# Kernel optimization log

Measured on AMD Instinct MI355X. Metric: run time of the kernel, lower is better.

## Reference

```python
import jax, jax.numpy as jnp
import numpy as np

B, N, CS, CZ, CH, H, PQ, PV = 1, 768, 384, 128, 16, 12, 4, 8
INF, EPS = 1e5, 1e-8


def quat_to_rot(q):
    q = q / jnp.linalg.norm(q, axis=-1, keepdims=True)
    w, x, y, z = q[..., 0], q[..., 1], q[..., 2], q[..., 3]
    r0 = jnp.stack([1 - 2 * (y * y + z * z), 2 * (x * y - w * z), 2 * (x * z + w * y)], -1)
    r1 = jnp.stack([2 * (x * y + w * z), 1 - 2 * (x * x + z * z), 2 * (y * z - w * x)], -1)
    r2 = jnp.stack([2 * (x * z - w * y), 2 * (y * z + w * x), 1 - 2 * (x * x + y * y)], -1)
    return jnp.stack([r0, r1, r2], -2)


def setup_inputs() -> dict:
    key = jax.random.key(0)
    ks = jax.random.split(key, 12)
    nrm = lambda k, shp, sc=1.0: jax.random.normal(k, shp, jnp.float32) * sc
    s = nrm(ks[0], (B, N, CS))
    z = nrm(ks[1], (B, N, N, CZ))
    rot = quat_to_rot(nrm(ks[2], (B, N, 4)))
    trans = nrm(ks[3], (B, N, 3))
    mask = jnp.ones((B, N), jnp.float32)
    dout = H * (CZ + CH + PV * 4)
    return dict(
        s=s, z=z, rot=rot, trans=trans, mask=mask,
        w_q=nrm(ks[4], (H * CH, CS), 0.02), b_q=jnp.zeros((H * CH,), jnp.float32),
        w_kv=nrm(ks[5], (2 * H * CH, CS), 0.02), b_kv=jnp.zeros((2 * H * CH,), jnp.float32),
        w_qp=nrm(ks[6], (H * PQ * 3, CS), 0.02), b_qp=jnp.zeros((H * PQ * 3,), jnp.float32),
        w_kvp=nrm(ks[7], (H * (PQ + PV) * 3, CS), 0.02), b_kvp=jnp.zeros((H * (PQ + PV) * 3,), jnp.float32),
        w_b=nrm(ks[8], (H, CZ), 0.02), b_b=jnp.zeros((H,), jnp.float32),
        head_weights=jnp.full((H,), 0.541324854612918, jnp.float32),
        w_out=nrm(ks[9], (CS, dout), 0.02), b_out=jnp.zeros((CS,), jnp.float32),
    )


def ipa_forward(s, z, rot, trans, mask, w_q, b_q, w_kv, b_kv, w_qp, b_qp,
                w_kvp, b_kvp, w_b, b_b, head_weights, w_out, b_out):
    # scalar q/k/v: [B,N,H,CH]
    q = (s @ w_q.T + b_q).reshape(B, N, H, CH)
    kv = (s @ w_kv.T + b_kv).reshape(B, N, H, 2 * CH)
    k, v = kv[..., :CH], kv[..., CH:]
    # point projections in local frame, then rigid apply: x_glob = R x + t
    qp = (s @ w_qp.T + b_qp).reshape(B, N, H, PQ, 3)
    kvp = (s @ w_kvp.T + b_kvp).reshape(B, N, H, PQ + PV, 3)
    t = trans[:, :, None, None, :]
    q_pts = jnp.einsum('bnij,bnhpj->bnhpi', rot, qp) + t
    kv_pts = jnp.einsum('bnij,bnhpj->bnhpi', rot, kvp) + t
    k_pts, v_pts = kv_pts[..., :PQ, :], kv_pts[..., PQ:, :]
    # pair bias: [B,H,N,N]
    b = jnp.moveaxis(z @ w_b.T + b_b, -1, 1)
    # scalar attention logits
    a = jnp.einsum('bihc,bjhc->bhij', q, k) * np.sqrt(1.0 / (3 * CH))
    a = a + np.sqrt(1.0 / 3) * b
    # point-distance attention: [B,N,N,H]
    diff = q_pts[:, :, None] - k_pts[:, None]  # [B,N,N,H,PQ,3]
    d2 = jnp.sum(diff * diff, axis=-1)  # [B,N,N,H,PQ]
    hw = jax.nn.softplus(head_weights) * np.sqrt(1.0 / (3 * (PQ * 9.0 / 2)))
    pt_att = -0.5 * jnp.sum(d2 * hw[None, None, None, :, None], axis=-1)
    a = a + jnp.moveaxis(pt_att, -1, 1)
    # mask
    sq_mask = INF * (mask[:, :, None] * mask[:, None, :] - 1.0)  # [B,N,N]
    a = jax.nn.softmax(a + sq_mask[:, None], axis=-1)  # [B,H,N,N]
    # outputs
    o = jnp.einsum('bhij,bjhc->bihc', a, v).reshape(B, N, H * CH)
    o_pt = jnp.einsum('bhij,bjhpx->bihpx', a, v_pts)  # global frame
    o_pt_loc = jnp.einsum('bnji,bnhpj->bnhpi', rot, o_pt - t)  # R^T (x - t)
    o_pt_norm = jnp.sqrt(jnp.sum(o_pt_loc * o_pt_loc, axis=-1) + EPS)  # [B,N,H,PV]
    o_pair = jnp.einsum('bhij,bijc->bihc', a, z).reshape(B, N, H * CZ)
    cat = jnp.concatenate([o, o_pt_loc.reshape(B, N, H * PV * 3),
                           o_pt_norm.reshape(B, N, H * PV), o_pair], axis=-1)
    return cat @ w_out.T + b_out  # [B,N,CS]


def reference(s, z, rot, trans, mask, w_q, b_q, w_kv, b_kv, w_qp, b_qp,
              w_kvp, b_kvp, w_b, b_b, head_weights, w_out, b_out):
    return ipa_forward(s, z, rot, trans, mask, w_q, b_q, w_kv, b_kv, w_qp, b_qp,
                       w_kvp, b_kvp, w_b, b_b, head_weights, w_out, b_out)
```

## Files before the change

### kernel.cpp

```cpp
#include <hip/hip_runtime.h>
#include <math.h>

#define Nn 768
#define NN 589824
#define DOUT 2112

#define WS_Q   0
#define WS_K   147456
#define WS_QP  442368
#define WS_KP  552960
#define WS_A   2506752
#define WS_VT  6045696
#define WS_CH  6230016
#define WS_CL  7041024
#define WS_WH  7852032
#define WS_WL  8257536

typedef unsigned short u16;
typedef unsigned int u32;

using bf16x8 = __attribute__((ext_vector_type(8))) short;
using f32x4  = __attribute__((ext_vector_type(4))) float;

__device__ __forceinline__ float bf2f(u16 u) {
  union { float f; u32 i; } x; x.i = ((u32)u) << 16; return x.f;
}
__device__ __forceinline__ u16 f2bf(float f) {
  union { float f; u32 i; } x; x.f = f;
  u32 r = x.i + 0x7FFFu + ((x.i >> 16) & 1u);
  return (u16)(r >> 16);
}
__device__ __forceinline__ void wr_hl(u16* ch, u16* cl, int idx, float v) {
  u16 hb = f2bf(v);
  ch[idx] = hb;
  cl[idx] = f2bf(v - bf2f(hb));
}

__global__ __launch_bounds__(256) void k_proj(
    const float* __restrict__ s, const float* __restrict__ rot, const float* __restrict__ trans,
    const float* __restrict__ w_q, const float* __restrict__ b_q,
    const float* __restrict__ w_kv, const float* __restrict__ b_kv,
    const float* __restrict__ w_qp, const float* __restrict__ b_qp,
    const float* __restrict__ w_kvp, const float* __restrict__ b_kvp,
    float* __restrict__ ws)
{
  __shared__ float s16[16][384];
  __shared__ float praw[16][192];
  __shared__ float rot16[16][9];
  __shared__ float t16[16][3];
  const int t = threadIdx.x;
  const int ib = blockIdx.x, fg = blockIdx.y;
  const int i0 = ib * 16;
  u16* VT = (u16*)(ws + WS_VT);

  {
    const float4* sp = (const float4*)(s + (size_t)i0 * 384);
    float4* dp = (float4*)&s16[0][0];
    for (int idx = t; idx < 1536; idx += 256) dp[idx] = sp[idx];
  }
  if (fg >= 3) {
    if (t < 144) rot16[t / 9][t % 9] = rot[i0 * 9 + t];
    else if (t < 192) { int g = t - 144; t16[g / 3][g % 3] = trans[i0 * 3 + g]; }
  }
  __syncthreads();

  const int rg = t >> 6;
  const int fl = t & 63;
  for (int p = 0; p < 3; p++) {
    const int f_loc = p * 64 + fl;
    const int F = fg * 192 + f_loc;
    const float* wrow; float bias;
    if (F < 192)      { wrow = w_q   + (size_t)F * 384;          bias = b_q[F]; }
    else if (F < 576) { int g = F - 192; wrow = w_kv  + (size_t)g * 384; bias = b_kv[g]; }
    else if (F < 720) { int g = F - 576; wrow = w_qp  + (size_t)g * 384; bias = b_qp[g]; }
    else              { int g = F - 720; wrow = w_kvp + (size_t)g * 384; bias = b_kvp[g]; }
    float a0 = bias, a1 = bias, a2 = bias, a3 = bias;
    const float4* w4 = (const float4*)wrow;
    #pragma unroll 4
    for (int c4 = 0; c4 < 96; c4++) {
      float4 wv = w4[c4];
      const float4 v0 = *(const float4*)&s16[rg * 4 + 0][c4 * 4];
      const float4 v1 = *(const float4*)&s16[rg * 4 + 1][c4 * 4];
      const float4 v2 = *(const float4*)&s16[rg * 4 + 2][c4 * 4];
      const float4 v3 = *(const float4*)&s16[rg * 4 + 3][c4 * 4];
      a0 += wv.x * v0.x + wv.y * v0.y + wv.z * v0.z + wv.w * v0.w;
      a1 += wv.x * v1.x + wv.y * v1.y + wv.z * v1.z + wv.w * v1.w;
      a2 += wv.x * v2.x + wv.y * v2.y + wv.z * v2.z + wv.w * v2.w;
      a3 += wv.x * v3.x + wv.y * v3.y + wv.z * v3.z + wv.w * v3.w;
    }
    float av[4] = {a0, a1, a2, a3};
    if (F < 576) {
      if (F < 192) {
        float* base = ws + WS_Q + ((F >> 4) * Nn) * 16 + (F & 15);
        #pragma unroll
        for (int r = 0; r < 4; r++) base[(i0 + rg * 4 + r) * 16] = av[r];
      } else {
        int g = F - 192, hh = g >> 5, x = g & 31;
        if (x < 16) {
          float* base = ws + WS_K + (hh * Nn) * 16 + x;
          #pragma unroll
          for (int r = 0; r < 4; r++) base[(i0 + rg * 4 + r) * 16] = av[r];
        } else {
          u16* vt = VT + (size_t)(hh * 40 + (x - 16)) * 768;
          #pragma unroll
          for (int r = 0; r < 4; r++) vt[i0 + rg * 4 + r] = f2bf(av[r]);
        }
      }
    } else {
      #pragma unroll
      for (int r = 0; r < 4; r++) praw[rg * 4 + r][f_loc] = av[r];
    }
  }
  if (fg >= 3) {
    __syncthreads();
    #pragma unroll
    for (int k = 0; k < 4; k++) {
      int tk = t + k * 256;
      int row = tk >> 6, tri = tk & 63;
      int g3 = tri * 3;
      int i = i0 + row;
      float vx = praw[row][g3], vy = praw[row][g3 + 1], vz = praw[row][g3 + 2];
      const float* R = rot16[row];
      const float* T = t16[row];
      float o0 = R[0] * vx + R[1] * vy + R[2] * vz + T[0];
      float o1 = R[3] * vx + R[4] * vy + R[5] * vz + T[1];
      float o2 = R[6] * vx + R[7] * vy + R[8] * vz + T[2];
      int pt_g = (fg - 3) * 192 + g3;
      if (pt_g < 144) {
        int hh = pt_g / 12, pp = (pt_g / 3) & 3;
        float* dst = ws + WS_QP + (hh * Nn + i) * 12 + pp * 3;
        dst[0] = o0; dst[1] = o1; dst[2] = o2;
      } else {
        int gg = pt_g - 144; int hh = gg / 36, pp = (gg / 3) % 12;
        if (pp < 4) {
          float* dst = ws + WS_KP + (hh * Nn + i) * 12 + pp * 3;
          dst[0] = o0; dst[1] = o1; dst[2] = o2;
        } else {
          u16* vt = VT + (size_t)(hh * 40 + 16 + (pp - 4) * 3) * 768 + i;
          vt[0] = f2bf(o0); vt[768] = f2bf(o1); vt[1536] = f2bf(o2);
        }
      }
    }
  }
}

__global__ __launch_bounds__(256) void k_bias(
    const float* __restrict__ z, const float* __restrict__ w_b, const float* __restrict__ b_b,
    u16* __restrict__ A)
{
  __shared__ float wb[12][128];
  __shared__ float bb[12];
  const int t = threadIdx.x;
  for (int idx = t; idx < 1536; idx += 256) wb[idx >> 7][idx & 127] = w_b[idx];
  if (t < 12) bb[t] = b_b[t];
  __syncthreads();
  const size_t pair = (size_t)blockIdx.x * 256 + t;
  const float4* zp = (const float4*)(z + pair * 128);
  float acc[12];
  #pragma unroll
  for (int h = 0; h < 12; h++) acc[h] = 0.f;
  #pragma unroll 4
  for (int c4 = 0; c4 < 32; c4++) {
    float4 zv = zp[c4];
    #pragma unroll
    for (int h = 0; h < 12; h++) {
      const float4 wv = *(const float4*)&wb[h][c4 * 4];
      acc[h] += zv.x * wv.x + zv.y * wv.y + zv.z * wv.z + zv.w * wv.w;
    }
  }
  #pragma unroll
  for (int h = 0; h < 12; h++) A[(size_t)h * NN + pair] = f2bf(acc[h] + bb[h]);
}

__global__ __launch_bounds__(256) void k_attn(
    const float* __restrict__ ws, u16* __restrict__ A,
    const float* __restrict__ mask, const float* __restrict__ head_weights)
{
  const int h = blockIdx.x;
  const int i0 = blockIdx.y * 4;
  const int t = threadIdx.x;
  const int lane = t & 63, wv = t >> 6;
  __shared__ float qrow[4][16];
  __shared__ float qp4[4][12];
  __shared__ float mi4[4];
  __shared__ float red[4][4];
  __shared__ float Msh[4], Ssh[4];

  if (t < 64) { int r = t >> 4, c = t & 15; qrow[r][c] = ws[WS_Q + (h * Nn + i0 + r) * 16 + c]; }
  else if (t < 112) { int g = t - 64; int r = g / 12, d = g - r * 12; qp4[r][d] = ws[WS_QP + (h * Nn + i0 + r) * 12 + d]; }
  else if (t < 116) mi4[t - 112] = mask[i0 + t - 112];
  const float hw = log1pf(__expf(head_weights[h]));
  const float cpt = -0.5f * hw * 0.13608276348795434f;
  __syncthreads();

  float L[4][3];
  float lmax[4] = {-1e30f, -1e30f, -1e30f, -1e30f};
  #pragma unroll
  for (int jj = 0; jj < 3; jj++) {
    const int j = t + jj * 256;
    const float4* kp = (const float4*)(ws + WS_K + (size_t)(h * Nn + j) * 16);
    float kr[16];
    #pragma unroll
    for (int u = 0; u < 4; u++) { float4 vv = kp[u]; kr[u*4] = vv.x; kr[u*4+1] = vv.y; kr[u*4+2] = vv.z; kr[u*4+3] = vv.w; }
    const float4* pp4 = (const float4*)(ws + WS_KP + (size_t)(h * Nn + j) * 12);
    float kpt[12];
    #pragma unroll
    for (int u = 0; u < 3; u++) { float4 vv = pp4[u]; kpt[u*4] = vv.x; kpt[u*4+1] = vv.y; kpt[u*4+2] = vv.z; kpt[u*4+3] = vv.w; }
    const float mj = mask[j];
    #pragma unroll
    for (int r = 0; r < 4; r++) {
      float qk = 0.f;
      #pragma unroll
      for (int c = 0; c < 16; c++) qk += qrow[r][c] * kr[c];
      float d2 = 0.f;
      #pragma unroll
      for (int d = 0; d < 12; d++) { float df = qp4[r][d] - kpt[d]; d2 += df * df; }
      float bias = bf2f(A[h * NN + (i0 + r) * Nn + j]);
      float Lv = qk * 0.14433756729740643f + 0.57735026918962584f * bias + cpt * d2
               + 100000.0f * (mi4[r] * mj - 1.0f);
      L[r][jj] = Lv;
      lmax[r] = fmaxf(lmax[r], Lv);
    }
  }
  #pragma unroll
  for (int r = 0; r < 4; r++) {
    float v = lmax[r];
    #pragma unroll
    for (int o = 32; o > 0; o >>= 1) v = fmaxf(v, __shfl_xor(v, o));
    if (lane == 0) red[wv][r] = v;
  }
  __syncthreads();
  if (t < 4) Msh[t] = fmaxf(fmaxf(red[0][t], red[1][t]), fmaxf(red[2][t], red[3][t]));
  __syncthreads();
  float lsum[4] = {0.f, 0.f, 0.f, 0.f};
  #pragma unroll
  for (int jj = 0; jj < 3; jj++) {
    #pragma unroll
    for (int r = 0; r < 4; r++) {
      float e = __expf(L[r][jj] - Msh[r]);
      L[r][jj] = e; lsum[r] += e;
    }
  }
  #pragma unroll
  for (int r = 0; r < 4; r++) {
    float v = lsum[r];
    #pragma unroll
    for (int o = 32; o > 0; o >>= 1) v += __shfl_xor(v, o);
    if (lane == 0) red[wv][r] = v;
  }
  __syncthreads();
  if (t < 4) Ssh[t] = red[0][t] + red[1][t] + red[2][t] + red[3][t];
  __syncthreads();
  float inv[4];
  #pragma unroll
  for (int r = 0; r < 4; r++) inv[r] = 1.0f / Ssh[r];
  #pragma unroll
  for (int jj = 0; jj < 3; jj++) {
    int j = t + jj * 256;
    #pragma unroll
    for (int r = 0; r < 4; r++)
      A[h * NN + (i0 + r) * Nn + j] = f2bf(L[r][jj] * inv[r]);
  }
}

__global__ __launch_bounds__(192) void k_out_ov(
    const u16* __restrict__ A, const u16* __restrict__ VT,
    const float* __restrict__ rot, const float* __restrict__ trans,
    float* __restrict__ ws)
{
  const int ib = blockIdx.x, h = blockIdx.y;
  const int i0 = ib * 16;
  const int t = threadIdx.x;
  const int w = t >> 6, lane = t & 63;
  const int n = lane & 15, quad = lane >> 4;
  __shared__ float opt[16][26];
  u16* CH = (u16*)(ws + WS_CH);
  u16* CL = (u16*)(ws + WS_CL);

  const int col40 = w * 16 + n;
  const bool bvalid = col40 < 40;
  const u16* abase = A + (size_t)h * NN + (size_t)(i0 + n) * Nn + quad * 8;
  const u16* bbase = VT + (size_t)(h * 40 + (bvalid ? col40 : 0)) * 768 + quad * 8;

  f32x4 acc = {0.f, 0.f, 0.f, 0.f};
  #pragma unroll 4
  for (int kk = 0; kk < 24; kk++) {
    bf16x8 af = *(const bf16x8*)(abase + kk * 32);
    bf16x8 bf = *(const bf16x8*)(bbase + kk * 32);
    if (!bvalid) bf = bf16x8{0, 0, 0, 0, 0, 0, 0, 0};
    acc = __builtin_amdgcn_mfma_f32_16x16x32_bf16(af, bf, acc, 0, 0, 0);
  }

  const int mrow = quad * 4;
  if (w == 0) {
    u16* chb = CH + (size_t)i0 * DOUT + h * 16 + n;
    u16* clb = CL + (size_t)i0 * DOUT + h * 16 + n;
    #pragma unroll
    for (int r = 0; r < 4; r++) wr_hl(chb, clb, (mrow + r) * DOUT, acc[r]);
  } else if (w == 1 || n < 8) {
    const int col = (w - 1) * 16 + n;
    #pragma unroll
    for (int r = 0; r < 4; r++) opt[mrow + r][col] = acc[r];
  }
  __syncthreads();
  if (t < 128) {
    const int ii = t >> 3, p = t & 7;
    const int i = i0 + ii;
    float R[9], T[3];
    #pragma unroll
    for (int u = 0; u < 9; u++) R[u] = rot[i * 9 + u];
    #pragma unroll
    for (int u = 0; u < 3; u++) T[u] = trans[i * 3 + u];
    float g0 = opt[ii][p * 3 + 0] - T[0];
    float g1 = opt[ii][p * 3 + 1] - T[1];
    float g2 = opt[ii][p * 3 + 2] - T[2];
    float lx = R[0] * g0 + R[3] * g1 + R[6] * g2;
    float ly = R[1] * g0 + R[4] * g1 + R[7] * g2;
    float lz = R[2] * g0 + R[5] * g1 + R[8] * g2;
    u16* chb = CH + (size_t)i * DOUT;
    u16* clb = CL + (size_t)i * DOUT;
    wr_hl(chb, clb, 192 + (h * 8 + p) * 3 + 0, lx);
    wr_hl(chb, clb, 192 + (h * 8 + p) * 3 + 1, ly);
    wr_hl(chb, clb, 192 + (h * 8 + p) * 3 + 2, lz);
    wr_hl(chb, clb, 480 + h * 8 + p, sqrtf(lx * lx + ly * ly + lz * lz + 1e-8f));
  }
}

__global__ __launch_bounds__(256) void k_out_pair(
    const float* __restrict__ z, const u16* __restrict__ A, float* __restrict__ ws)
{
  const int i = blockIdx.x;
  const int t = threadIdx.x;
  __shared__ u16 aL[12 * 768];
  __shared__ float zch[16][128];
  __shared__ float af[12][16];
  const int c = t & 127, grp = t >> 7;

  for (int idx = t; idx < 4608; idx += 256) {
    int hh = idx / 384, u = idx - hh * 384;
    ((u32*)aL)[hh * 384 + u] = ((const u32*)(A + (size_t)hh * NN + i * Nn))[u];
  }
  float acc[6];
  #pragma unroll
  for (int hh = 0; hh < 6; hh++) acc[hh] = 0.f;

  const float4* zsrc = (const float4*)(z + (size_t)i * Nn * 128);
  float4 p0 = zsrc[t], p1 = zsrc[t + 256];

  for (int jb = 0; jb < 48; jb++) {
    __syncthreads();
    {
      int i0x = t, i1x = t + 256;
      *(float4*)&zch[i0x >> 5][(i0x & 31) * 4] = p0;
      *(float4*)&zch[i1x >> 5][(i1x & 31) * 4] = p1;
    }
    if (t < 192) af[t >> 4][t & 15] = bf2f(aL[(t >> 4) * 768 + jb * 16 + (t & 15)]);
    __syncthreads();
    if (jb + 1 < 48) {
      const float4* zn = zsrc + (size_t)(jb + 1) * 512;
      p0 = zn[t]; p1 = zn[t + 256];
    }
    #pragma unroll 4
    for (int r = 0; r < 16; r++) {
      float zv = zch[r][c];
      #pragma unroll
      for (int hh = 0; hh < 6; hh++)
        acc[hh] += af[grp * 6 + hh][r] * zv;
    }
  }
  u16* chb = (u16*)(ws + WS_CH) + (size_t)i * DOUT + 576;
  u16* clb = (u16*)(ws + WS_CL) + (size_t)i * DOUT + 576;
  #pragma unroll
  for (int hh = 0; hh < 6; hh++)
    wr_hl(chb, clb, (grp * 6 + hh) * 128 + c, acc[hh]);
}

__global__ __launch_bounds__(256) void k_wcvt(const float* __restrict__ w_out, float* __restrict__ ws)
{
  const int idx = blockIdx.x * 256 + threadIdx.x;
  float4 v = ((const float4*)w_out)[idx];
  u16 h0 = f2bf(v.x), h1 = f2bf(v.y), h2 = f2bf(v.z), h3 = f2bf(v.w);
  ushort4 hv; hv.x = h0; hv.y = h1; hv.z = h2; hv.w = h3;
  ushort4 lv;
  lv.x = f2bf(v.x - bf2f(h0));
  lv.y = f2bf(v.y - bf2f(h1));
  lv.z = f2bf(v.z - bf2f(h2));
  lv.w = f2bf(v.w - bf2f(h3));
  ((ushort4*)(ws + WS_WH))[idx] = hv;
  ((ushort4*)(ws + WS_WL))[idx] = lv;
}

__global__ __launch_bounds__(256) void k_final_mfma(
    const float* __restrict__ ws, const float* __restrict__ b_out, float* __restrict__ outp)
{
  const int i0 = blockIdx.x * 16, c0 = blockIdx.y * 16;
  const int t = threadIdx.x;
  const int w = t >> 6, lane = t & 63;
  const int n = lane & 15, quad = lane >> 4;
  const u16* CH  = (const u16*)(ws + WS_CH);
  const u16* CL  = (const u16*)(ws + WS_CL);
  const u16* WHp = (const u16*)(ws + WS_WH);
  const u16* WLp = (const u16*)(ws + WS_WL);
  const u16* ah_p = CH  + (size_t)(i0 + n) * DOUT + quad * 8;
  const u16* al_p = CL  + (size_t)(i0 + n) * DOUT + quad * 8;
  const u16* bh_p = WHp + (size_t)(c0 + n) * DOUT + quad * 8;
  const u16* bl_p = WLp + (size_t)(c0 + n) * DOUT + quad * 8;

  const int s0 = (w * 66) >> 2, s1 = ((w + 1) * 66) >> 2;
  f32x4 acc = {0.f, 0.f, 0.f, 0.f};
  for (int ss = s0; ss < s1; ss++) {
    bf16x8 ah = *(const bf16x8*)(ah_p + ss * 32);
    bf16x8 al = *(const bf16x8*)(al_p + ss * 32);
    bf16x8 bh = *(const bf16x8*)(bh_p + ss * 32);
    bf16x8 bl = *(const bf16x8*)(bl_p + ss * 32);
    acc = __builtin_amdgcn_mfma_f32_16x16x32_bf16(ah, bh, acc, 0, 0, 0);
    acc = __builtin_amdgcn_mfma_f32_16x16x32_bf16(ah, bl, acc, 0, 0, 0);
    acc = __builtin_amdgcn_mfma_f32_16x16x32_bf16(al, bh, acc, 0, 0, 0);
  }

  __shared__ float red[4][64][4];
  #pragma unroll
  for (int r = 0; r < 4; r++) red[w][lane][r] = acc[r];
  __syncthreads();
  if (w == 0) {
    const float bo = b_out[c0 + n];
    #pragma unroll
    for (int r = 0; r < 4; r++) {
      float v = red[0][lane][r] + red[1][lane][r] + red[2][lane][r] + red[3][lane][r] + bo;
      outp[(size_t)(i0 + quad * 4 + r) * 384 + c0 + n] = v;
    }
  }
}

extern "C" void kernel_launch(void* const* d_in, const int* in_sizes, int n_in,
                              void* d_out, int out_size, void* d_ws, size_t ws_size,
                              hipStream_t stream)
{
  const float* s      = (const float*)d_in[0];
  const float* z      = (const float*)d_in[1];
  const float* rot    = (const float*)d_in[2];
  const float* trans  = (const float*)d_in[3];
  const float* mask   = (const float*)d_in[4];
  const float* w_q    = (const float*)d_in[5];
  const float* b_q    = (const float*)d_in[6];
  const float* w_kv   = (const float*)d_in[7];
  const float* b_kv   = (const float*)d_in[8];
  const float* w_qp   = (const float*)d_in[9];
  const float* b_qp   = (const float*)d_in[10];
  const float* w_kvp  = (const float*)d_in[11];
  const float* b_kvp  = (const float*)d_in[12];
  const float* w_b    = (const float*)d_in[13];
  const float* b_b    = (const float*)d_in[14];
  const float* hwts   = (const float*)d_in[15];
  const float* w_out  = (const float*)d_in[16];
  const float* b_out  = (const float*)d_in[17];
  float* ws = (float*)d_ws;
  u16* A = (u16*)(ws + WS_A);
  u16* VT = (u16*)(ws + WS_VT);
  float* outp = (float*)d_out;

  k_wcvt<<<dim3(792), dim3(256), 0, stream>>>(w_out, ws);
  k_proj<<<dim3(48, 6), dim3(256), 0, stream>>>(s, rot, trans, w_q, b_q, w_kv, b_kv,
                                                w_qp, b_qp, w_kvp, b_kvp, ws);
  k_bias<<<dim3(2304), dim3(256), 0, stream>>>(z, w_b, b_b, A);
  k_attn<<<dim3(12, 192), dim3(256), 0, stream>>>(ws, A, mask, hwts);
  k_out_ov<<<dim3(48, 12), dim3(192), 0, stream>>>(A, VT, rot, trans, ws);
  k_out_pair<<<dim3(768), dim3(256), 0, stream>>>(z, A, ws);
  k_final_mfma<<<dim3(48, 24), dim3(256), 0, stream>>>(ws, b_out, outp);
}
```

Baseline: 669.7 us.

## Compute pair-output aggregation with bf16 MFMA using hi/lo split of z

Rewrites k_out_pair to use 16x16x32 bf16 MFMA instructions instead of LDS-staged scalar FMAs. z is split into bf16 high and low parts so accuracy stays near fp32, and the attention rows are loaded straight from global memory. The 16-row MFMA tile covers 12 heads, so four rows read data past the head range and are then discarded. Separately, k_bias drops its shared-memory staging of w_b and reads the weights and bias directly from global memory. The new z loads are scalar and strided rather than float4, which could hurt coalescing.

```diff
diff --git a/kernel.cpp b/kernel.cpp
--- a/kernel.cpp
+++ b/kernel.cpp
@@ -148,28 +148,24 @@
     const float* __restrict__ z, const float* __restrict__ w_b, const float* __restrict__ b_b,
     u16* __restrict__ A)
 {
-  __shared__ float wb[12][128];
-  __shared__ float bb[12];
-  const int t = threadIdx.x;
-  for (int idx = t; idx < 1536; idx += 256) wb[idx >> 7][idx & 127] = w_b[idx];
-  if (t < 12) bb[t] = b_b[t];
-  __syncthreads();
+  const int t = threadIdx.x;
   const size_t pair = (size_t)blockIdx.x * 256 + t;
   const float4* zp = (const float4*)(z + pair * 128);
+  const float4* wb4 = (const float4*)w_b;
   float acc[12];
   #pragma unroll
-  for (int h = 0; h < 12; h++) acc[h] = 0.f;
+  for (int h = 0; h < 12; h++) acc[h] = b_b[h];
   #pragma unroll 4
   for (int c4 = 0; c4 < 32; c4++) {
     float4 zv = zp[c4];
     #pragma unroll
     for (int h = 0; h < 12; h++) {
-      const float4 wv = *(const float4*)&wb[h][c4 * 4];
+      const float4 wv = wb4[h * 32 + c4];
       acc[h] += zv.x * wv.x + zv.y * wv.y + zv.z * wv.z + zv.w * wv.w;
     }
   }
   #pragma unroll
-  for (int h = 0; h < 12; h++) A[(size_t)h * NN + pair] = f2bf(acc[h] + bb[h]);
+  for (int h = 0; h < 12; h++) A[(size_t)h * NN + pair] = f2bf(acc[h]);
 }
 
 __global__ __launch_bounds__(256) void k_attn(
@@ -331,48 +327,52 @@
 {
   const int i = blockIdx.x;
   const int t = threadIdx.x;
-  __shared__ u16 aL[12 * 768];
-  __shared__ float zch[16][128];
-  __shared__ float af[12][16];
-  const int c = t & 127, grp = t >> 7;
-
-  for (int idx = t; idx < 4608; idx += 256) {
-    int hh = idx / 384, u = idx - hh * 384;
-    ((u32*)aL)[hh * 384 + u] = ((const u32*)(A + (size_t)hh * NN + i * Nn))[u];
-  }
-  float acc[6];
-  #pragma unroll
-  for (int hh = 0; hh < 6; hh++) acc[hh] = 0.f;
-
-  const float4* zsrc = (const float4*)(z + (size_t)i * Nn * 128);
-  float4 p0 = zsrc[t], p1 = zsrc[t + 256];
-
-  for (int jb = 0; jb < 48; jb++) {
-    __syncthreads();
-    {
-      int i0x = t, i1x = t + 256;
-      *(float4*)&zch[i0x >> 5][(i0x & 31) * 4] = p0;
-      *(float4*)&zch[i1x >> 5][(i1x & 31) * 4] = p1;
-    }
-    if (t < 192) af[t >> 4][t & 15] = bf2f(aL[(t >> 4) * 768 + jb * 16 + (t & 15)]);
-    __syncthreads();
-    if (jb + 1 < 48) {
-      const float4* zn = zsrc + (size_t)(jb + 1) * 512;
-      p0 = zn[t]; p1 = zn[t + 256];
-    }
-    #pragma unroll 4
-    for (int r = 0; r < 16; r++) {
-      float zv = zch[r][c];
-      #pragma unroll
-      for (int hh = 0; hh < 6; hh++)
-        acc[hh] += af[grp * 6 + hh][r] * zv;
-    }
-  }
-  u16* chb = (u16*)(ws + WS_CH) + (size_t)i * DOUT + 576;
-  u16* clb = (u16*)(ws + WS_CL) + (size_t)i * DOUT + 576;
-  #pragma unroll
-  for (int hh = 0; hh < 6; hh++)
-    wr_hl(chb, clb, (grp * 6 + hh) * 128 + c, acc[hh]);
+  const int w = t >> 6, lane = t & 63;
+  const int x = lane & 15, quad = lane >> 4;
+  u16* CH = (u16*)(ws + WS_CH);
+  u16* CL = (u16*)(ws + WS_CL);
+
+  const u16* ap = A + (size_t)x * NN + (size_t)i * Nn + quad * 8;
+  const float* zrow = z + (size_t)i * Nn * 128;
+  const int c0a = (w * 2) * 16 + x;
+  const int c0b = (w * 2 + 1) * 16 + x;
+
+  f32x4 accA = {0.f, 0.f, 0.f, 0.f};
+  f32x4 accB = {0.f, 0.f, 0.f, 0.f};
+  #pragma unroll 2
+  for (int ks = 0; ks < 24; ks++) {
+    bf16x8 af = *(const bf16x8*)(ap + ks * 32);
+    const float* zb = zrow + (size_t)(ks * 32 + quad * 8) * 128;
+    float va[8], vb[8];
+    #pragma unroll
+    for (int j = 0; j < 8; j++) {
+      va[j] = zb[j * 128 + c0a];
+      vb[j] = zb[j * 128 + c0b];
+    }
+    bf16x8 zah, zal, zbh, zbl;
+    #pragma unroll
+    for (int j = 0; j < 8; j++) {
+      u16 h0 = f2bf(va[j]);
+      zah[j] = (short)h0; zal[j] = (short)f2bf(va[j] - bf2f(h0));
+      u16 h1 = f2bf(vb[j]);
+      zbh[j] = (short)h1; zbl[j] = (short)f2bf(vb[j] - bf2f(h1));
+    }
+    accA = __builtin_amdgcn_mfma_f32_16x16x32_bf16(af, zah, accA, 0, 0, 0);
+    accA = __builtin_amdgcn_mfma_f32_16x16x32_bf16(af, zal, accA, 0, 0, 0);
+    accB = __builtin_amdgcn_mfma_f32_16x16x32_bf16(af, zbh, accB, 0, 0, 0);
+    accB = __builtin_amdgcn_mfma_f32_16x16x32_bf16(af, zbl, accB, 0, 0, 0);
+  }
+
+  if (quad < 3) {
+    u16* chb = CH + (size_t)i * DOUT + 576;
+    u16* clb = CL + (size_t)i * DOUT + 576;
+    #pragma unroll
+    for (int r = 0; r < 4; r++) {
+      const int head = quad * 4 + r;
+      wr_hl(chb, clb, head * 128 + c0a, accA[r]);
+      wr_hl(chb, clb, head * 128 + c0b, accB[r]);
+    }
+  }
 }
 
 __global__ __launch_bounds__(256) void k_wcvt(const float* __restrict__ w_out, float* __restrict__ ws)
```

New measurement: 668.5 us. Within noise of the previous version (-0.2%).
